# Optimization experiments

Hardware: AMD Instinct MI355X
Metric: run time of the kernel (lower is better)

The kernel has to match this reference:

```python
import jax, jax.numpy as jnp
import numpy as np

B, NI, NA, D = 16, 2048, 2048, 256

def setup_inputs() -> dict:
    key = jax.random.key(0)
    k1, k2, k3 = jax.random.split(key, 3)
    input_seq = jax.random.normal(k1, (B, NI, D), dtype=jnp.float32)
    attendee_seq = jax.random.normal(k2, (B, NA, D), dtype=jnp.float32)
    # glorot-ish scale for bilinear weight
    W = jax.random.normal(k3, (D, D), dtype=jnp.float32) * (1.0 / np.sqrt(D))
    return {"input_seq": input_seq, "attendee_seq": attendee_seq, "W": W}

def reference(input_seq, attendee_seq, W):
    # bilinear scores: (x_i W) . a_j   -> [B, NI, NA]
    xW = jnp.einsum('bid,de->bie', input_seq, W)
    scores = jnp.einsum('bie,bje->bij', xW, attendee_seq)
    A = jax.nn.softmax(scores, axis=2)                 # softmax over attendee axis
    # weighted context: sum_j A[b,i,j] * v[b,j,:] -> [B, NI, D]
    attended = jnp.einsum('bij,bjd->bid', A, attendee_seq)
    return attended
```

## Files before the change

### kernel.cpp

```cpp
#include <hip/hip_runtime.h>
#include <hip/hip_bf16.h>

#define BB 16
#define NI 2048
#define NA 2048
#define DD 256
#define KVB 32
#define NT (NA / KVB)

typedef _Float16 half8 __attribute__((ext_vector_type(8)));
typedef _Float16 half2t __attribute__((ext_vector_type(2)));
typedef __attribute__((ext_vector_type(4))) float f32x4;
typedef __attribute__((ext_vector_type(4))) unsigned int uint4v;

typedef const unsigned int CGU __attribute__((address_space(1)));
typedef unsigned int LU __attribute__((address_space(3)));

static __device__ __forceinline__ unsigned short f2h(float f) {
  union { _Float16 h; unsigned short u; } x; x.h = (_Float16)f; return x.u;
}
static __device__ __forceinline__ float h2f(unsigned short u) {
  union { _Float16 h; unsigned short u; } x; x.u = u; return (float)x.h;
}
static __device__ __forceinline__ unsigned int pk2(float a, float b) {
  return __builtin_bit_cast(unsigned int, __builtin_amdgcn_cvt_pkrtz(a, b));
}
static __device__ __forceinline__ void gload16(const unsigned short* g, unsigned short* l) {
  __builtin_amdgcn_global_load_lds((CGU*)g, (LU*)l, 16, 0, 0);
}

__global__ void prep_kernel(const float* __restrict__ a,
                            unsigned short* __restrict__ kfrag,
                            unsigned short* __restrict__ vfrag,
                            const float* __restrict__ w,
                            unsigned short* __restrict__ wth,
                            unsigned short* __restrict__ wtl) {
  __shared__ float t[64][65];
  int bx = blockIdx.x;
  int tid = threadIdx.x;
  int rr = tid >> 4, c4 = tid & 15;

  if (bx >= 2048) {
    int r = bx - 2048;
    int dt = r >> 2, et = r & 3;
    int d0 = dt * 64, e0 = et * 64;
    int cc = c4 * 4;
#pragma unroll
    for (int k = 0; k < 4; ++k) {
      int row = rr + k * 16;
      float4 v = *(const float4*)(w + (size_t)(d0 + row) * DD + e0 + cc);
      t[row][cc + 0] = v.x; t[row][cc + 1] = v.y; t[row][cc + 2] = v.z; t[row][cc + 3] = v.w;
    }
    __syncthreads();
#pragma unroll
    for (int k = 0; k < 4; ++k) {
      int e = rr + k * 16;
      int eg = e0 + e;
      ushort4 h, l;
      float v0 = t[cc + 0][e]; h.x = f2h(v0); l.x = f2h(v0 - h2f(h.x));
      float v1 = t[cc + 1][e]; h.y = f2h(v1); l.y = f2h(v1 - h2f(h.y));
      float v2 = t[cc + 2][e]; h.z = f2h(v2); l.z = f2h(v2 - h2f(h.z));
      float v3 = t[cc + 3][e]; h.w = f2h(v3); l.w = f2h(v3 - h2f(h.w));
      int dd = d0 + cc;
      int u = dd >> 3, sub = dd & 7;
      size_t off = (size_t)eg * DD + ((u ^ (eg & 7)) * 8) + sub;
      *(ushort4*)(wth + off) = h;
      *(ushort4*)(wtl + off) = l;
    }
    return;
  }

  int b = bx >> 7;
  int r = bx & 127;
  int jt_t = r >> 2, dt_t = r & 3;
  int j0 = jt_t * 64, d0 = dt_t * 64;
#pragma unroll
  for (int k = 0; k < 4; ++k) {
    int row = rr + k * 16;
    int j = j0 + row;
    int d = d0 + c4 * 4;
    float4 v = *(const float4*)(a + ((size_t)b * NA + j) * DD + d);
    ushort4 hh;
    hh.x = f2h(v.x); hh.y = f2h(v.y); hh.z = f2h(v.z); hh.w = f2h(v.w);
    int kt = j >> 5, jtf = (j >> 4) & 1, l16k = j & 15;
    int c = d >> 5, quad = (d >> 3) & 3, e = d & 7;
    *(ushort4*)(kfrag + ((size_t)b * NT + kt) * 8192 + c * 1024 + jtf * 512 +
                (quad * 16 + l16k) * 8 + e) = hh;
    t[row][c4 * 4 + 0] = v.x; t[row][c4 * 4 + 1] = v.y;
    t[row][c4 * 4 + 2] = v.z; t[row][c4 * 4 + 3] = v.w;
  }
  __syncthreads();
#pragma unroll
  for (int k = 0; k < 4; ++k) {
    int dl = rr + k * 16;
    int d = d0 + dl;
    int j = j0 + c4 * 4;
    ushort4 o;
    o.x = f2h(t[c4 * 4 + 0][dl]); o.y = f2h(t[c4 * 4 + 1][dl]);
    o.z = f2h(t[c4 * 4 + 2][dl]); o.w = f2h(t[c4 * 4 + 3][dl]);
    int kt = j >> 5;
    int quad = c4 & 3;
    int jt = (c4 >> 2) & 1;
    int hh_ = (d >> 7) & 1, dtl = (d >> 4) & 7, l16v = d & 15;
    *(ushort4*)(vfrag + ((size_t)b * NT + kt) * 8192 + hh_ * 4096 + dtl * 512 +
                (quad * 16 + l16v) * 8 + jt * 4) = o;
  }
}

__global__ __launch_bounds__(256, 2) void qgemm_kernel(
    const float* __restrict__ x, const unsigned short* __restrict__ wth,
    const unsigned short* __restrict__ wtl, unsigned short* __restrict__ qf) {
  __shared__ unsigned short wb[2][64 * 256];
  const int tid = threadIdx.x;
  const int lane = tid & 63;
  const int wv = tid >> 6;
  const int quad = lane >> 4;
  const int l16 = lane & 15;
  const int m0 = blockIdx.x * 64;

  half8 xf[8];
  {
    const float* xr = x + (size_t)(m0 + wv * 16 + l16) * DD;
#pragma unroll
    for (int c = 0; c < 8; ++c) {
      float4 a = *(const float4*)(xr + c * 32 + quad * 8);
      float4 b = *(const float4*)(xr + c * 32 + quad * 8 + 4);
      half8 v;
      v[0] = (_Float16)a.x; v[1] = (_Float16)a.y; v[2] = (_Float16)a.z; v[3] = (_Float16)a.w;
      v[4] = (_Float16)b.x; v[5] = (_Float16)b.y; v[6] = (_Float16)b.z; v[7] = (_Float16)b.w;
      xf[c] = v;
    }
  }

#pragma unroll 1
  for (int eg = 0; eg < 4; ++eg) {
    uint4 t0[8], t1[8];
    {
      const unsigned short* sh = wth + (size_t)(eg * 64) * DD;
      const unsigned short* sl = wtl + (size_t)(eg * 64) * DD;
#pragma unroll
      for (int i = 0; i < 8; ++i) {
        t0[i] = *(const uint4*)(sh + (i * 256 + tid) * 8);
        t1[i] = *(const uint4*)(sl + (i * 256 + tid) * 8);
      }
    }
    __syncthreads();
#pragma unroll
    for (int i = 0; i < 8; ++i) {
      *(uint4*)(wb[0] + (i * 256 + tid) * 8) = t0[i];
      *(uint4*)(wb[1] + (i * 256 + tid) * 8) = t1[i];
    }
    __syncthreads();
#pragma unroll
    for (int etl = 0; etl < 4; ++etl) {
      int rloc = etl * 16 + l16;
      f32x4 acc; acc[0] = acc[1] = acc[2] = acc[3] = 0.f;
#pragma unroll
      for (int c = 0; c < 8; ++c) {
        int off = rloc * DD + (((4 * c + quad) ^ (rloc & 7)) * 8);
        half8 wh = *(const half8*)(wb[0] + off);
        half8 wl = *(const half8*)(wb[1] + off);
        acc = __builtin_amdgcn_mfma_f32_16x16x32_f16(xf[c], wh, acc, 0, 0, 0);
        acc = __builtin_amdgcn_mfma_f32_16x16x32_f16(xf[c], wl, acc, 0, 0, 0);
      }
      int e = eg * 64 + etl * 16 + l16;
#pragma unroll
      for (int rg = 0; rg < 4; ++rg) {
        qf[(size_t)(m0 + wv * 16 + 4 * quad + rg) * DD + e] = f2h(acc[rg] * 1.44269504f);
      }
    }
  }
}

__global__ __launch_bounds__(256, 4) void attn_kernel(
    const unsigned short* __restrict__ kfrag, const unsigned short* __restrict__ vfrag,
    const unsigned short* __restrict__ qf, float* __restrict__ out) {
  __shared__ unsigned short kls[2][KVB * DD];
  __shared__ uint2 sx[2][2][2][64];

  const int tid = threadIdx.x;
  const int lane = tid & 63;
  const int wv = tid >> 6;
  const int p = wv >> 1;
  const int h = wv & 1;
  const int quad = lane >> 4;
  const int l16 = lane & 15;

  int bx = blockIdx.x;
  int lbx = (bx & 7) * 128 + (bx >> 3);
  const int b = lbx >> 6;
  const int qbase = (lbx & 63) * 32 + p * 16;

  const unsigned short* kfb = kfrag + (size_t)b * NT * 8192;
  const unsigned short* vfb = vfrag + (size_t)b * NT * 8192 + h * 4096;

  half8 qh[8];
  {
    const size_t qrow = ((size_t)b * NI + qbase + l16) * DD;
#pragma unroll
    for (int c = 0; c < 8; ++c)
      qh[c] = *(const half8*)(qf + qrow + c * 32 + quad * 8);
  }

  f32x4 acc[8];
#pragma unroll
  for (int dt = 0; dt < 8; ++dt) { acc[dt][0] = 0.f; acc[dt][1] = 0.f; acc[dt][2] = 0.f; acc[dt][3] = 0.f; }
  float m0r = -INFINITY;
  float l0 = 0.f;

#pragma unroll
  for (int i = 0; i < 4; ++i) {
    int off = (i * 4 + wv) * 512;
    gload16(kfb + off + lane * 8, &kls[0][off]);
  }
  __syncthreads();

#pragma unroll 1
  for (int kt = 0; kt < NT; ++kt) {
    half8 vb[8];
#pragma unroll
    for (int dt = 0; dt < 8; ++dt)
      vb[dt] = *(const half8*)(vfb + (size_t)kt * 8192 + dt * 512 + lane * 8);

    if (kt + 1 < NT) {
      const unsigned short* s = kfb + (size_t)(kt + 1) * 8192;
      unsigned short* d = &kls[(kt + 1) & 1][0];
#pragma unroll
      for (int i = 0; i < 4; ++i) {
        int off = (i * 4 + wv) * 512;
        gload16(s + off + lane * 8, d + off);
      }
    }

    const unsigned short* kb = &kls[kt & 1][0];
    f32x4 sa, sb;
    sa[0]=sa[1]=sa[2]=sa[3]=0.f; sb[0]=sb[1]=sb[2]=sb[3]=0.f;
    __builtin_amdgcn_s_setprio(1);
#pragma unroll
    for (int c = 0; c < 4; ++c) {
      half8 k0 = *(const half8*)(kb + c * 1024 + h * 512 + lane * 8);
      sa = __builtin_amdgcn_mfma_f32_16x16x32_f16(k0, qh[c], sa, 0, 0, 0);
    }
#pragma unroll
    for (int c = 4; c < 8; ++c) {
      half8 k0 = *(const half8*)(kb + c * 1024 + h * 512 + lane * 8);
      sb = __builtin_amdgcn_mfma_f32_16x16x32_f16(k0, qh[c], sb, 0, 0, 0);
    }
    __builtin_amdgcn_s_setprio(0);
    f32x4 s;
    s[0] = sa[0] + sb[0]; s[1] = sa[1] + sb[1];
    s[2] = sa[2] + sb[2]; s[3] = sa[3] + sb[3];

    sx[kt & 1][p][h][lane] = make_uint2(pk2(s[0], s[1]), pk2(s[2], s[3]));
    __syncthreads();

    uint2 ox = sx[kt & 1][p][h ^ 1][lane];
    half2t oa = __builtin_bit_cast(half2t, ox.x);
    half2t ob = __builtin_bit_cast(half2t, ox.y);
    float o0 = (float)oa[0], o1 = (float)oa[1];
    float o2 = (float)ob[0], o3 = (float)ob[1];

    float mt = fmaxf(fmaxf(fmaxf(s[0], s[1]), fmaxf(s[2], s[3])),
                     fmaxf(fmaxf(o0, o1), fmaxf(o2, o3)));
    if (__any(mt > m0r + 11.5416f)) {
      float mr = fmaxf(mt, __shfl_xor(mt, 16));
      mr = fmaxf(mr, __shfl_xor(mr, 32));
      float mn = fmaxf(m0r, mr);
      float sc = exp2f(m0r - mn);
      l0 *= sc;
#pragma unroll
      for (int rg = 0; rg < 4; ++rg) {
        float a0 = __shfl(sc, 4 * quad + rg);
#pragma unroll
        for (int dt = 0; dt < 8; ++dt) acc[dt][rg] *= a0;
      }
      m0r = mn;
    }

    float es0 = exp2f(s[0] - m0r), es1 = exp2f(s[1] - m0r);
    float es2 = exp2f(s[2] - m0r), es3 = exp2f(s[3] - m0r);
    float eo0 = exp2f(o0 - m0r), eo1 = exp2f(o1 - m0r);
    float eo2 = exp2f(o2 - m0r), eo3 = exp2f(o3 - m0r);
    l0 += ((es0 + es1) + (es2 + es3)) + ((eo0 + eo1) + (eo2 + eo3));
    unsigned int d0 = pk2(es0, es1), d1 = pk2(es2, es3);
    unsigned int c0 = pk2(eo0, eo1), c1 = pk2(eo2, eo3);
    uint4v pau;
    if (h == 0) { pau[0] = d0; pau[1] = d1; pau[2] = c0; pau[3] = c1; }
    else        { pau[0] = c0; pau[1] = c1; pau[2] = d0; pau[3] = d1; }
    half8 pa = __builtin_bit_cast(half8, pau);

    __builtin_amdgcn_s_setprio(1);
#pragma unroll
    for (int dt = 0; dt < 8; ++dt)
      acc[dt] = __builtin_amdgcn_mfma_f32_16x16x32_f16(pa, vb[dt], acc[dt], 0, 0, 0);
    __builtin_amdgcn_s_setprio(0);
  }

  l0 += __shfl_xor(l0, 16); l0 += __shfl_xor(l0, 32);
  float inv0 = 1.0f / l0;
  size_t ob = ((size_t)b * NI + qbase) * DD + h * 128;
#pragma unroll
  for (int rg = 0; rg < 4; ++rg) {
    float i0 = __shfl(inv0, 4 * quad + rg);
#pragma unroll
    for (int dt = 0; dt < 8; ++dt) {
      int d = dt * 16 + l16;
      out[ob + (size_t)(4 * quad + rg) * DD + d] = acc[dt][rg] * i0;
    }
  }
}

extern "C" void kernel_launch(void* const* d_in, const int* in_sizes, int n_in,
                              void* d_out, int out_size, void* d_ws, size_t ws_size,
                              hipStream_t stream) {
  const float* x = (const float*)d_in[0];
  const float* att = (const float*)d_in[1];
  const float* W = (const float*)d_in[2];
  float* out = (float*)d_out;

  const size_t NE = (size_t)BB * NA * DD;
  unsigned short* w0    = (unsigned short*)d_ws;
  unsigned short* kfrag = w0;
  unsigned short* vfrag = w0 + NE;
  unsigned short* qfp   = w0 + 2 * NE;
  unsigned short* wth   = w0 + 3 * NE;
  unsigned short* wtl   = w0 + 3 * NE + (size_t)DD * DD;

  prep_kernel<<<2064, 256, 0, stream>>>(att, kfrag, vfrag, W, wth, wtl);
  qgemm_kernel<<<512, 256, 0, stream>>>(x, wth, wtl, qfp);
  attn_kernel<<<1024, 256, 0, stream>>>(kfrag, vfrag, qfp, out);
}
```

Measured before the change: 196.5 us.

## Software-pipeline attention loop: defer softmax and PV of tile kt-1

Restructures the main KV loop so the softmax and P·V MFMAs for the previous tile run after the QK MFMAs of the current tile, before the barrier, instead of waiting on a barrier mid-iteration. Score exchange between the two half-waves now uses fp32 values in a doubled shared buffer, and an epilogue handles the final tile. The aim is to hide the barrier and exchange latency behind independent MFMA work. It costs more shared memory and registers (held previous scores and V fragments), which may lower occupancy. The V loads now fetch the previous tile's data, so they no longer arrive ahead of use.

```diff
diff --git a/kernel.cpp b/kernel.cpp
--- a/kernel.cpp
+++ b/kernel.cpp
@@ -9,7 +9,6 @@
 #define NT (NA / KVB)
 
 typedef _Float16 half8 __attribute__((ext_vector_type(8)));
-typedef _Float16 half2t __attribute__((ext_vector_type(2)));
 typedef __attribute__((ext_vector_type(4))) float f32x4;
 typedef __attribute__((ext_vector_type(4))) unsigned int uint4v;
 
@@ -24,6 +23,12 @@
 }
 static __device__ __forceinline__ unsigned int pk2(float a, float b) {
   return __builtin_bit_cast(unsigned int, __builtin_amdgcn_cvt_pkrtz(a, b));
+}
+static __device__ __forceinline__ unsigned int f2u(float f) {
+  return __builtin_bit_cast(unsigned int, f);
+}
+static __device__ __forceinline__ float u2f(unsigned int u) {
+  return __builtin_bit_cast(float, u);
 }
 static __device__ __forceinline__ void gload16(const unsigned short* g, unsigned short* l) {
   __builtin_amdgcn_global_load_lds((CGU*)g, (LU*)l, 16, 0, 0);
@@ -176,7 +181,7 @@
     const unsigned short* __restrict__ kfrag, const unsigned short* __restrict__ vfrag,
     const unsigned short* __restrict__ qf, float* __restrict__ out) {
   __shared__ unsigned short kls[2][KVB * DD];
-  __shared__ uint2 sx[2][2][2][64];
+  __shared__ uint4 sx[2][2][2][64];
 
   const int tid = threadIdx.x;
   const int lane = tid & 63;
@@ -207,6 +212,7 @@
   for (int dt = 0; dt < 8; ++dt) { acc[dt][0] = 0.f; acc[dt][1] = 0.f; acc[dt][2] = 0.f; acc[dt][3] = 0.f; }
   float m0r = -INFINITY;
   float l0 = 0.f;
+  f32x4 sprev;
 
 #pragma unroll
   for (int i = 0; i < 4; ++i) {
@@ -218,9 +224,11 @@
 #pragma unroll 1
   for (int kt = 0; kt < NT; ++kt) {
     half8 vb[8];
-#pragma unroll
-    for (int dt = 0; dt < 8; ++dt)
-      vb[dt] = *(const half8*)(vfb + (size_t)kt * 8192 + dt * 512 + lane * 8);
+    if (kt > 0) {
+#pragma unroll
+      for (int dt = 0; dt < 8; ++dt)
+        vb[dt] = *(const half8*)(vfb + (size_t)(kt - 1) * 8192 + dt * 512 + lane * 8);
+    }
 
     if (kt + 1 < NT) {
       const unsigned short* s = kfb + (size_t)(kt + 1) * 8192;
@@ -251,16 +259,59 @@
     s[0] = sa[0] + sb[0]; s[1] = sa[1] + sb[1];
     s[2] = sa[2] + sb[2]; s[3] = sa[3] + sb[3];
 
-    sx[kt & 1][p][h][lane] = make_uint2(pk2(s[0], s[1]), pk2(s[2], s[3]));
+    sx[kt & 1][p][h][lane] = make_uint4(f2u(s[0]), f2u(s[1]), f2u(s[2]), f2u(s[3]));
+
+    if (kt > 0) {
+      uint4 ox = sx[(kt - 1) & 1][p][h ^ 1][lane];
+      float o0 = u2f(ox.x), o1 = u2f(ox.y), o2 = u2f(ox.z), o3 = u2f(ox.w);
+
+      float mt = fmaxf(fmaxf(fmaxf(sprev[0], sprev[1]), fmaxf(sprev[2], sprev[3])),
+                       fmaxf(fmaxf(o0, o1), fmaxf(o2, o3)));
+      if (__any(mt > m0r + 11.5416f)) {
+        float mr = fmaxf(mt, __shfl_xor(mt, 16));
+        mr = fmaxf(mr, __shfl_xor(mr, 32));
+        float mn = fmaxf(m0r, mr);
+        float sc = exp2f(m0r - mn);
+        l0 *= sc;
+#pragma unroll
+        for (int rg = 0; rg < 4; ++rg) {
+          float a0 = __shfl(sc, 4 * quad + rg);
+#pragma unroll
+          for (int dt = 0; dt < 8; ++dt) acc[dt][rg] *= a0;
+        }
+        m0r = mn;
+      }
+
+      float es0 = exp2f(sprev[0] - m0r), es1 = exp2f(sprev[1] - m0r);
+      float es2 = exp2f(sprev[2] - m0r), es3 = exp2f(sprev[3] - m0r);
+      float eo0 = exp2f(o0 - m0r), eo1 = exp2f(o1 - m0r);
+      float eo2 = exp2f(o2 - m0r), eo3 = exp2f(o3 - m0r);
+      l0 += ((es0 + es1) + (es2 + es3)) + ((eo0 + eo1) + (eo2 + eo3));
+      unsigned int d0 = pk2(es0, es1), d1 = pk2(es2, es3);
+      unsigned int c0 = pk2(eo0, eo1), c1 = pk2(eo2, eo3);
+      uint4v pau;
+      if (h == 0) { pau[0] = d0; pau[1] = d1; pau[2] = c0; pau[3] = c1; }
+      else        { pau[0] = c0; pau[1] = c1; pau[2] = d0; pau[3] = d1; }
+      half8 pa = __builtin_bit_cast(half8, pau);
+
+      __builtin_amdgcn_s_setprio(1);
+#pragma unroll
+      for (int dt = 0; dt < 8; ++dt)
+        acc[dt] = __builtin_amdgcn_mfma_f32_16x16x32_f16(pa, vb[dt], acc[dt], 0, 0, 0);
+      __builtin_amdgcn_s_setprio(0);
+    }
+    sprev = s;
     __syncthreads();
-
-    uint2 ox = sx[kt & 1][p][h ^ 1][lane];
-    half2t oa = __builtin_bit_cast(half2t, ox.x);
-    half2t ob = __builtin_bit_cast(half2t, ox.y);
-    float o0 = (float)oa[0], o1 = (float)oa[1];
-    float o2 = (float)ob[0], o3 = (float)ob[1];
-
-    float mt = fmaxf(fmaxf(fmaxf(s[0], s[1]), fmaxf(s[2], s[3])),
+  }
+
+  {
+    half8 vb[8];
+#pragma unroll
+    for (int dt = 0; dt < 8; ++dt)
+      vb[dt] = *(const half8*)(vfb + (size_t)(NT - 1) * 8192 + dt * 512 + lane * 8);
+    uint4 ox = sx[(NT - 1) & 1][p][h ^ 1][lane];
+    float o0 = u2f(ox.x), o1 = u2f(ox.y), o2 = u2f(ox.z), o3 = u2f(ox.w);
+    float mt = fmaxf(fmaxf(fmaxf(sprev[0], sprev[1]), fmaxf(sprev[2], sprev[3])),
                      fmaxf(fmaxf(o0, o1), fmaxf(o2, o3)));
     if (__any(mt > m0r + 11.5416f)) {
       float mr = fmaxf(mt, __shfl_xor(mt, 16));
@@ -276,9 +327,8 @@
       }
       m0r = mn;
     }
-
-    float es0 = exp2f(s[0] - m0r), es1 = exp2f(s[1] - m0r);
-    float es2 = exp2f(s[2] - m0r), es3 = exp2f(s[3] - m0r);
+    float es0 = exp2f(sprev[0] - m0r), es1 = exp2f(sprev[1] - m0r);
+    float es2 = exp2f(sprev[2] - m0r), es3 = exp2f(sprev[3] - m0r);
     float eo0 = exp2f(o0 - m0r), eo1 = exp2f(o1 - m0r);
     float eo2 = exp2f(o2 - m0r), eo3 = exp2f(o3 - m0r);
     l0 += ((es0 + es1) + (es2 + es3)) + ((eo0 + eo1) + (eo2 + eo3));
@@ -288,12 +338,9 @@
     if (h == 0) { pau[0] = d0; pau[1] = d1; pau[2] = c0; pau[3] = c1; }
     else        { pau[0] = c0; pau[1] = c1; pau[2] = d0; pau[3] = d1; }
     half8 pa = __builtin_bit_cast(half8, pau);
-
-    __builtin_amdgcn_s_setprio(1);
 #pragma unroll
     for (int dt = 0; dt < 8; ++dt)
       acc[dt] = __builtin_amdgcn_mfma_f32_16x16x32_f16(pa, vb[dt], acc[dt], 0, 0, 0);
-    __builtin_amdgcn_s_setprio(0);
   }
 
   l0 += __shfl_xor(l0, 16); l0 += __shfl_xor(l0, 32);
```

After: 211.4 us. +7.5%, slower.
